# Optimization experiments

Measured on AMD Instinct MI355X. Metric: run time of the kernel, lower is better.

The kernel has to match this reference:

```python
import jax, jax.numpy as jnp
import numpy as np

D_IN = 1024
D_OUT = 1024
NUM_HEADS = 16
D_HEAD = D_OUT // NUM_HEADS


def setup_inputs() -> dict:
    key = jax.random.key(0)
    ks = jax.random.split(key, 6)
    s = 0.02
    return {
        "x": jax.random.normal(ks[0], (2, 2048, D_IN), dtype=jnp.float32),
        "W_q": jax.random.normal(ks[1], (D_IN, D_OUT), dtype=jnp.float32) * s,
        "W_k": jax.random.normal(ks[2], (D_IN, D_OUT), dtype=jnp.float32) * s,
        "W_v": jax.random.normal(ks[3], (D_IN, D_OUT), dtype=jnp.float32) * s,
        "W_o": jax.random.normal(ks[4], (D_OUT, D_OUT), dtype=jnp.float32) * s,
        "b_o": jax.random.normal(ks[5], (D_OUT,), dtype=jnp.float32) * s,
    }


def reference(x, W_q, W_k, W_v, W_o, b_o):
    B, T, _ = x.shape
    # qkv projections (no bias), split heads -> [B, H, T, d_head]
    def split_heads(t):
        return t.reshape(B, T, NUM_HEADS, D_HEAD).transpose(0, 2, 1, 3)
    q = split_heads(x @ W_q)
    k = split_heads(x @ W_k)
    v = split_heads(x @ W_v)
    # full causal scores [B, H, T, T]
    scores = jnp.einsum("bhqd,bhkd->bhqk", q, k)
    causal = jnp.triu(jnp.ones((T, T), dtype=bool), k=1)
    scores = jnp.where(causal, -jnp.inf, scores)
    attn = jax.nn.softmax(scores / np.sqrt(D_HEAD).astype(np.float32), axis=-1)
    # dropout rate is 0.0 -> identity
    ctx = jnp.einsum("bhqk,bhkd->bhqd", attn, v)
    ctx = ctx.transpose(0, 2, 1, 3).reshape(B, T, D_OUT)
    return ctx @ W_o + b_o
```

## Files before the change

kernel.cpp:

```cpp
#include <hip/hip_runtime.h>
#include <hip/hip_bf16.h>
#include <cstdint>

#define SEQ_T 2048
#define DMODEL 1024
#define NHEAD 16
#define DHEAD 64

typedef __attribute__((ext_vector_type(8))) __bf16 bf16x8;
typedef __attribute__((ext_vector_type(4))) float floatx4;

static __device__ __forceinline__ uint16_t f2bf(float f) {
    union { float f; uint32_t u; } v; v.f = f;
    uint32_t r = v.u + 0x7FFFu + ((v.u >> 16) & 1u);
    return (uint16_t)(r >> 16);
}

__global__ void mha_cvt_x(const float* __restrict__ x, uint16_t* __restrict__ xb) {
    int i = (blockIdx.x * blockDim.x + threadIdx.x) * 4;
    float4 f = *(const float4*)(x + i);
    union { uint16_t u[4]; uint64_t v; } o;
    o.u[0] = f2bf(f.x); o.u[1] = f2bf(f.y); o.u[2] = f2bf(f.z); o.u[3] = f2bf(f.w);
    *(uint64_t*)(xb + i) = o.v;
}

__global__ void mha_cvt_wt(const float* __restrict__ W0, const float* __restrict__ W1,
                           const float* __restrict__ W2, const float* __restrict__ W3,
                           uint16_t* __restrict__ T0, uint16_t* __restrict__ T1,
                           uint16_t* __restrict__ T2, uint16_t* __restrict__ T3) {
    const float* W; uint16_t* Tt;
    switch (blockIdx.z) {
        case 0: W = W0; Tt = T0; break;
        case 1: W = W1; Tt = T1; break;
        case 2: W = W2; Tt = T2; break;
        default: W = W3; Tt = T3; break;
    }
    __shared__ float tile[64][65];
    const int c  = threadIdx.x & 63;
    const int r0 = threadIdx.x >> 6;
    const int R0 = blockIdx.y * 64, C0 = blockIdx.x * 64;
#pragma unroll
    for (int rr = 0; rr < 16; ++rr) {
        int r = r0 + rr * 4;
        tile[r][c] = W[(size_t)(R0 + r) * DMODEL + C0 + c];
    }
    __syncthreads();
#pragma unroll
    for (int rr = 0; rr < 16; ++rr) {
        int r = r0 + rr * 4;
        Tt[(size_t)(C0 + r) * DMODEL + R0 + c] = f2bf(tile[c][r]);
    }
}

template<int MODE>
__device__ __forceinline__ void gemm128_body(
    const uint16_t* __restrict__ A, const uint16_t* __restrict__ Bt,
    uint16_t* __restrict__ outB) {
    const int K = DMODEL, N = DMODEL;
    __shared__ uint16_t As[128 * 32];
    __shared__ uint16_t Bs[128 * 32];
    const int tid  = threadIdx.x;
    const int wave = tid >> 6;
    const int lane = tid & 63;
    const int m0 = blockIdx.y * 128;
    const int n0 = blockIdx.x * 128;
    const int lr   = lane & 15;
    const int quad = lane >> 4;
    const int wm = wave >> 1, wn = wave & 1;

    floatx4 acc[4][4];
#pragma unroll
    for (int i = 0; i < 4; ++i)
#pragma unroll
        for (int j = 0; j < 4; ++j) acc[i][j] = (floatx4)0.0f;

    for (int k0 = 0; k0 < K; k0 += 32) {
#pragma unroll
        for (int i = 0; i < 2; ++i) {
            int chunk = i * 256 + wave * 64 + lane;
            int r  = chunk >> 2;
            int c8 = (chunk & 3) * 8;
            const uint16_t* ga = A  + (size_t)(m0 + r) * K + k0 + c8;
            const uint16_t* gb = Bt + (size_t)(n0 + r) * K + k0 + c8;
            uint16_t* la = &As[(size_t)(i * 256 + wave * 64) * 8];
            uint16_t* lb = &Bs[(size_t)(i * 256 + wave * 64) * 8];
            __builtin_amdgcn_global_load_lds((const __attribute__((address_space(1))) void*)ga,
                                             (__attribute__((address_space(3))) void*)la, 16, 0, 0);
            __builtin_amdgcn_global_load_lds((const __attribute__((address_space(1))) void*)gb,
                                             (__attribute__((address_space(3))) void*)lb, 16, 0, 0);
        }
        __syncthreads();
        bf16x8 af[4], bfr[4];
#pragma unroll
        for (int mi = 0; mi < 4; ++mi)
            af[mi] = *(const bf16x8*)&As[(wm * 64 + mi * 16 + lr) * 32 + quad * 8];
#pragma unroll
        for (int ni = 0; ni < 4; ++ni)
            bfr[ni] = *(const bf16x8*)&Bs[(wn * 64 + ni * 16 + lr) * 32 + quad * 8];
#pragma unroll
        for (int mi = 0; mi < 4; ++mi)
#pragma unroll
            for (int ni = 0; ni < 4; ++ni)
                acc[mi][ni] = __builtin_amdgcn_mfma_f32_16x16x32_bf16(af[mi], bfr[ni], acc[mi][ni], 0, 0, 0);
        __syncthreads();
    }
    if constexpr (MODE == 1) {
        __shared__ uint16_t Ct[64][136];
        const int bb = m0 >> 11;
        const int t0 = m0 & 2047;
#pragma unroll
        for (int p = 0; p < 2; ++p) {
            if (wn == p) {
#pragma unroll
                for (int mi = 0; mi < 4; ++mi)
#pragma unroll
                    for (int ni = 0; ni < 4; ++ni) {
                        int cl = ni * 16 + lr;
                        int tl = wm * 64 + mi * 16 + quad * 4;
                        union { uint16_t u[4]; uint64_t v8; } pk;
#pragma unroll
                        for (int r = 0; r < 4; ++r) pk.u[r] = f2bf(acc[mi][ni][r]);
                        *(uint64_t*)&Ct[cl][tl] = pk.v8;
                    }
            }
            __syncthreads();
#pragma unroll
            for (int k = 0; k < 4; ++k) {
                int c  = k * 256 + tid;
                int cl = c >> 4;
                int off = (c & 15) * 8;
                uint4 v = *(const uint4*)&Ct[cl][off];
                *(uint4*)&outB[((size_t)(bb * 1024 + n0 + p * 64 + cl)) * 2048 + t0 + off] = v;
            }
            __syncthreads();
        }
    } else {
#pragma unroll
        for (int mi = 0; mi < 4; ++mi)
#pragma unroll
            for (int ni = 0; ni < 4; ++ni) {
                int col = n0 + wn * 64 + ni * 16 + lr;
#pragma unroll
                for (int r = 0; r < 4; ++r) {
                    int row = m0 + wm * 64 + mi * 16 + quad * 4 + r;
                    outB[(size_t)row * N + col] = f2bf(acc[mi][ni][r]);
                }
            }
    }
}

__global__ __launch_bounds__(256) void mha_gemm_qkv(
    const uint16_t* __restrict__ A,
    const uint16_t* __restrict__ Wq, const uint16_t* __restrict__ Wk, const uint16_t* __restrict__ Wv,
    uint16_t* __restrict__ Q, uint16_t* __restrict__ K, uint16_t* __restrict__ Vt) {
    switch (blockIdx.z) {
        case 0:  gemm128_body<0>(A, Wq, Q);  break;
        case 1:  gemm128_body<0>(A, Wk, K);  break;
        default: gemm128_body<1>(A, Wv, Vt); break;
    }
}

__global__ __launch_bounds__(256) void mha_gemm_out(
    const uint16_t* __restrict__ A, const uint16_t* __restrict__ Wot,
    float* __restrict__ out, const float* __restrict__ bias) {
    const int K = DMODEL, N = DMODEL;
    __shared__ uint16_t As[128 * 32];
    __shared__ uint16_t Bs[64 * 32];
    const int tid  = threadIdx.x;
    const int wave = tid >> 6;
    const int lane = tid & 63;
    const int m0 = blockIdx.y * 128;
    const int n0 = blockIdx.x * 64;
    const int lr   = lane & 15;
    const int quad = lane >> 4;
    const int wm = wave >> 1, wn = wave & 1;

    floatx4 acc[4][2];
#pragma unroll
    for (int i = 0; i < 4; ++i)
#pragma unroll
        for (int j = 0; j < 2; ++j) acc[i][j] = (floatx4)0.0f;

    for (int k0 = 0; k0 < K; k0 += 32) {
#pragma unroll
        for (int i = 0; i < 2; ++i) {
            int chunk = i * 256 + wave * 64 + lane;
            int r  = chunk >> 2;
            int c8 = (chunk & 3) * 8;
            const uint16_t* ga = A + (size_t)(m0 + r) * K + k0 + c8;
            uint16_t* la = &As[(size_t)(i * 256 + wave * 64) * 8];
            __builtin_amdgcn_global_load_lds((const __attribute__((address_space(1))) void*)ga,
                                             (__attribute__((address_space(3))) void*)la, 16, 0, 0);
        }
        {
            int chunk = wave * 64 + lane;
            int r  = chunk >> 2;
            int c8 = (chunk & 3) * 8;
            const uint16_t* gb = Wot + (size_t)(n0 + r) * K + k0 + c8;
            uint16_t* lb = &Bs[(size_t)(wave * 64) * 8];
            __builtin_amdgcn_global_load_lds((const __attribute__((address_space(1))) void*)gb,
                                             (__attribute__((address_space(3))) void*)lb, 16, 0, 0);
        }
        __syncthreads();
        bf16x8 af[4], bfr[2];
#pragma unroll
        for (int mi = 0; mi < 4; ++mi)
            af[mi] = *(const bf16x8*)&As[(wm * 64 + mi * 16 + lr) * 32 + quad * 8];
#pragma unroll
        for (int ni = 0; ni < 2; ++ni)
            bfr[ni] = *(const bf16x8*)&Bs[(wn * 32 + ni * 16 + lr) * 32 + quad * 8];
#pragma unroll
        for (int mi = 0; mi < 4; ++mi)
#pragma unroll
            for (int ni = 0; ni < 2; ++ni)
                acc[mi][ni] = __builtin_amdgcn_mfma_f32_16x16x32_bf16(af[mi], bfr[ni], acc[mi][ni], 0, 0, 0);
        __syncthreads();
    }
#pragma unroll
    for (int mi = 0; mi < 4; ++mi)
#pragma unroll
        for (int ni = 0; ni < 2; ++ni) {
            int col = n0 + wn * 32 + ni * 16 + lr;
            float bv = bias[col];
#pragma unroll
            for (int r = 0; r < 4; ++r) {
                int row = m0 + wm * 64 + mi * 16 + quad * 4 + r;
                out[(size_t)row * N + col] = acc[mi][ni][r] + bv;
            }
        }
}

__global__ __launch_bounds__(256) void mha_attn_mfma(
    const uint16_t* __restrict__ Q, const uint16_t* __restrict__ K,
    const uint16_t* __restrict__ Vt, uint16_t* __restrict__ ctx) {
    __shared__ alignas(16) uint16_t Ks[2][64 * 64];
    __shared__ alignas(16) uint16_t Vs[2][64 * 64];
    __shared__ alignas(16) uint16_t Pb[64 * 72];

    const int tid  = threadIdx.x;
    const int wave = tid >> 6;
    const int lane = tid & 63;
    const int lr   = lane & 15;
    const int quad = lane >> 4;
    const int p  = blockIdx.x;
    const int h  = blockIdx.y;
    const int b  = blockIdx.z;
    const int jH = 31 - p, jL = p;
    const int TH = jH + 1;
    const int TL = jL + 1;
    const int Ttot = TH + TL;

    const uint16_t* kbase[2];
    const uint16_t* vbase[2];
#pragma unroll
    for (int i = 0; i < 2; ++i) {
        int c = i * 256 + tid;
        int row = c >> 3, cs = c & 7;
        int csk = cs ^ (row & 7);
        kbase[i] = K  + ((size_t)(b * SEQ_T) + row) * DMODEL + h * DHEAD + csk * 8;
        vbase[i] = Vt + ((size_t)(b * 1024 + h * DHEAD + row)) * 2048 + csk * 8;
    }

    int wrow = jH * 64 + wave * 16;
    bf16x8 qf0, qf1;
    {
        const size_t qb = ((size_t)(b * SEQ_T) + wrow + lr) * DMODEL + h * DHEAD;
        qf0 = *(const bf16x8*)(Q + qb + quad * 8);
        qf1 = *(const bf16x8*)(Q + qb + 32 + quad * 8);
    }
    floatx4 o[4];
#pragma unroll
    for (int nt = 0; nt < 4; ++nt) o[nt] = (floatx4)0.0f;
    float l[4] = {0.f, 0.f, 0.f, 0.f};

    auto stage = [&](int kv0, int buf) {
#pragma unroll
        for (int i = 0; i < 2; ++i) {
            const uint16_t* gk = kbase[i] + (size_t)kv0 * DMODEL;
            const uint16_t* gv = vbase[i] + kv0;
            uint16_t* lk = &Ks[buf][(i * 256 + wave * 64) * 8];
            uint16_t* lv = &Vs[buf][(i * 256 + wave * 64) * 8];
            __builtin_amdgcn_global_load_lds((const __attribute__((address_space(1))) void*)gk,
                                             (__attribute__((address_space(3))) void*)lk, 16, 0, 0);
            __builtin_amdgcn_global_load_lds((const __attribute__((address_space(1))) void*)gv,
                                             (__attribute__((address_space(3))) void*)lv, 16, 0, 0);
        }
    };
    auto epilogue = [&]() {
#pragma unroll
        for (int r = 0; r < 4; ++r) {
            float v = l[r];
            v += __shfl_xor(v, 1, 64);
            v += __shfl_xor(v, 2, 64);
            v += __shfl_xor(v, 4, 64);
            v += __shfl_xor(v, 8, 64);
            l[r] = 1.f / v;
        }
#pragma unroll
        for (int nt = 0; nt < 4; ++nt)
#pragma unroll
            for (int r = 0; r < 4; ++r) {
                size_t addr = ((size_t)(b * SEQ_T) + wrow + quad * 4 + r) * DMODEL + h * DHEAD + nt * 16 + lr;
                ctx[addr] = f2bf(o[nt][r] * l[r]);
            }
    };

    stage(0, 0);
    __syncthreads();
    int cur = 0;

    for (int t = 0; t < Ttot; ++t) {
        if (t + 1 < Ttot) {
            int nkv0 = ((t + 1 < TH) ? (t + 1) : (t + 1 - TH)) * 64;
            stage(nkv0, cur ^ 1);
        }
        const int kv0 = ((t < TH) ? t : (t - TH)) * 64;

        floatx4 s[4];
#pragma unroll
        for (int nt = 0; nt < 4; ++nt) {
            s[nt] = (floatx4)0.0f;
            int krow = nt * 16 + lr;
#pragma unroll
            for (int ks = 0; ks < 2; ++ks) {
                bf16x8 kf = *(const bf16x8*)&Ks[cur][krow * 64 + (((ks * 4 + quad) ^ (lr & 7)) * 8)];
                s[nt] = __builtin_amdgcn_mfma_f32_16x16x32_bf16(ks ? qf1 : qf0, kf, s[nt], 0, 0, 0);
            }
        }
        if (kv0 + 63 > wrow) {
#pragma unroll
            for (int nt = 0; nt < 4; ++nt) {
                int kcol = kv0 + nt * 16 + lr;
#pragma unroll
                for (int r = 0; r < 4; ++r) {
                    int qrow = wrow + quad * 4 + r;
                    if (kcol > qrow) s[nt][r] = -3e38f;
                }
            }
        }
#pragma unroll
        for (int nt = 0; nt < 4; ++nt)
#pragma unroll
            for (int r = 0; r < 4; ++r) {
                float pe = __expf(s[nt][r] * 0.125f);
                uint32_t pu = __float_as_uint(pe);
                l[r] += __uint_as_float(pu & 0xffff0000u);
                Pb[(wave * 16 + quad * 4 + r) * 72 + nt * 16 + lr] = (uint16_t)(pu >> 16);
            }
#pragma unroll
        for (int ks = 0; ks < 2; ++ks) {
            bf16x8 pfr = *(const bf16x8*)&Pb[(wave * 16 + lr) * 72 + ks * 32 + quad * 8];
#pragma unroll
            for (int nt = 0; nt < 4; ++nt) {
                int vrow = nt * 16 + lr;
                bf16x8 vf = *(const bf16x8*)&Vs[cur][vrow * 64 + (((ks * 4 + quad) ^ (lr & 7)) * 8)];
                o[nt] = __builtin_amdgcn_mfma_f32_16x16x32_bf16(pfr, vf, o[nt], 0, 0, 0);
            }
        }
        if (t == TH - 1) {
            epilogue();
            wrow = jL * 64 + wave * 16;
            const size_t qb = ((size_t)(b * SEQ_T) + wrow + lr) * DMODEL + h * DHEAD;
            qf0 = *(const bf16x8*)(Q + qb + quad * 8);
            qf1 = *(const bf16x8*)(Q + qb + 32 + quad * 8);
#pragma unroll
            for (int nt = 0; nt < 4; ++nt) o[nt] = (floatx4)0.0f;
#pragma unroll
            for (int r = 0; r < 4; ++r) l[r] = 0.f;
        }
        __syncthreads();
        cur ^= 1;
    }
    epilogue();
}

extern "C" void kernel_launch(void* const* d_in, const int* in_sizes, int n_in,
                              void* d_out, int out_size, void* d_ws, size_t ws_size,
                              hipStream_t stream) {
    const float* x  = (const float*)d_in[0];
    const float* Wq = (const float*)d_in[1];
    const float* Wk = (const float*)d_in[2];
    const float* Wv = (const float*)d_in[3];
    const float* Wo = (const float*)d_in[4];
    const float* bo = (const float*)d_in[5];
    float* out = (float*)d_out;

    char* ws = (char*)d_ws;
    const size_t SZ_X = (size_t)4096 * DMODEL * 2;
    const size_t SZ_W = (size_t)DMODEL * DMODEL * 2;
    size_t off = 0;
    uint16_t* xb  = (uint16_t*)(ws + off); off += SZ_X;
    uint16_t* wqt = (uint16_t*)(ws + off); off += SZ_W;
    uint16_t* wkt = (uint16_t*)(ws + off); off += SZ_W;
    uint16_t* wvt = (uint16_t*)(ws + off); off += SZ_W;
    uint16_t* wot = (uint16_t*)(ws + off); off += SZ_W;
    uint16_t* Qb  = (uint16_t*)(ws + off); off += SZ_X;
    uint16_t* Kb  = (uint16_t*)(ws + off); off += SZ_X;
    uint16_t* Vtb = (uint16_t*)(ws + off); off += SZ_X;
    uint16_t* Cb  = (uint16_t*)(ws + off); off += SZ_X;
    (void)ws_size; (void)in_sizes; (void)n_in; (void)out_size;

    mha_cvt_x<<<4096, 256, 0, stream>>>(x, xb);
    mha_cvt_wt<<<dim3(16, 16, 4), 256, 0, stream>>>(Wq, Wk, Wv, Wo, wqt, wkt, wvt, wot);
    mha_gemm_qkv<<<dim3(8, 32, 3), 256, 0, stream>>>(xb, wqt, wkt, wvt, Qb, Kb, Vtb);
    mha_attn_mfma<<<dim3(16, NHEAD, 2), 256, 0, stream>>>(Qb, Kb, Vtb, Cb);
    mha_gemm_out<<<dim3(16, 32), 256, 0, stream>>>(Cb, wot, out, bo);
}
```

Before: 201.6 us.

## Shrink GEMM tiles for more blocks, add LDS swizzle, reorder attention grid

Cuts the QKV projection tile to 64x128 and the output projection tile to 64x64, which doubles the block count so the 256 CUs are better filled. Adds an XOR swizzle to the LDS layouts to reduce bank conflicts on the MFMA fragment reads and the V-transpose staging. Swaps the attention grid axes so heads become the fastest-varying index, changing block scheduling order. Smaller tiles lower per-block data reuse and raise global and L2 traffic.

After: 198.6 us. About the same (-1.5%).

```diff
diff --git a/kernel.cpp b/kernel.cpp
--- a/kernel.cpp
+++ b/kernel.cpp
@@ -53,96 +53,98 @@
 }
 
 template<int MODE>
-__device__ __forceinline__ void gemm128_body(
+__device__ __forceinline__ void gemm64x128_body(
     const uint16_t* __restrict__ A, const uint16_t* __restrict__ Bt,
     uint16_t* __restrict__ outB) {
     const int K = DMODEL, N = DMODEL;
-    __shared__ uint16_t As[128 * 32];
-    __shared__ uint16_t Bs[128 * 32];
+    __shared__ alignas(16) char smem[(MODE == 1) ? 18432 : 12288];
+    uint16_t* As = (uint16_t*)smem;
+    uint16_t* Bs = (uint16_t*)(smem + 4096);
     const int tid  = threadIdx.x;
     const int wave = tid >> 6;
     const int lane = tid & 63;
-    const int m0 = blockIdx.y * 128;
+    const int m0 = blockIdx.y * 64;
     const int n0 = blockIdx.x * 128;
     const int lr   = lane & 15;
     const int quad = lane >> 4;
-    const int wm = wave >> 1, wn = wave & 1;
-
-    floatx4 acc[4][4];
+
+    floatx4 acc[4][2];
 #pragma unroll
     for (int i = 0; i < 4; ++i)
 #pragma unroll
-        for (int j = 0; j < 4; ++j) acc[i][j] = (floatx4)0.0f;
+        for (int j = 0; j < 2; ++j) acc[i][j] = (floatx4)0.0f;
 
     for (int k0 = 0; k0 < K; k0 += 32) {
 #pragma unroll
-        for (int i = 0; i < 2; ++i) {
-            int chunk = i * 256 + wave * 64 + lane;
-            int r  = chunk >> 2;
-            int c8 = (chunk & 3) * 8;
-            const uint16_t* ga = A  + (size_t)(m0 + r) * K + k0 + c8;
-            const uint16_t* gb = Bt + (size_t)(n0 + r) * K + k0 + c8;
-            uint16_t* la = &As[(size_t)(i * 256 + wave * 64) * 8];
-            uint16_t* lb = &Bs[(size_t)(i * 256 + wave * 64) * 8];
-            __builtin_amdgcn_global_load_lds((const __attribute__((address_space(1))) void*)ga,
-                                             (__attribute__((address_space(3))) void*)la, 16, 0, 0);
-            __builtin_amdgcn_global_load_lds((const __attribute__((address_space(1))) void*)gb,
-                                             (__attribute__((address_space(3))) void*)lb, 16, 0, 0);
-        }
-        __syncthreads();
-        bf16x8 af[4], bfr[4];
+        for (int it = 0; it < 3; ++it) {
+            int c = it * 256 + wave * 64 + lane;
+            if (it == 0) {
+                int r = c >> 2, s = (c & 3) ^ ((r >> 1) & 3);
+                const uint16_t* g = A + (size_t)(m0 + r) * K + k0 + s * 8;
+                uint16_t* l = As + (size_t)c * 8;
+                __builtin_amdgcn_global_load_lds((const __attribute__((address_space(1))) void*)g,
+                                                 (__attribute__((address_space(3))) void*)l, 16, 0, 0);
+            } else {
+                int j = c - 256;
+                int r = j >> 2, s = (j & 3) ^ ((r >> 1) & 3);
+                const uint16_t* g = Bt + (size_t)(n0 + r) * K + k0 + s * 8;
+                uint16_t* l = Bs + (size_t)j * 8;
+                __builtin_amdgcn_global_load_lds((const __attribute__((address_space(1))) void*)g,
+                                                 (__attribute__((address_space(3))) void*)l, 16, 0, 0);
+            }
+        }
+        __syncthreads();
+        bf16x8 af[4], bfr[2];
+#pragma unroll
+        for (int mi = 0; mi < 4; ++mi) {
+            int row = mi * 16 + lr;
+            af[mi] = *(const bf16x8*)&As[row * 32 + ((quad ^ ((row >> 1) & 3)) << 3)];
+        }
+#pragma unroll
+        for (int ni = 0; ni < 2; ++ni) {
+            int row = wave * 32 + ni * 16 + lr;
+            bfr[ni] = *(const bf16x8*)&Bs[row * 32 + ((quad ^ ((row >> 1) & 3)) << 3)];
+        }
 #pragma unroll
         for (int mi = 0; mi < 4; ++mi)
-            af[mi] = *(const bf16x8*)&As[(wm * 64 + mi * 16 + lr) * 32 + quad * 8];
-#pragma unroll
-        for (int ni = 0; ni < 4; ++ni)
-            bfr[ni] = *(const bf16x8*)&Bs[(wn * 64 + ni * 16 + lr) * 32 + quad * 8];
+#pragma unroll
+            for (int ni = 0; ni < 2; ++ni)
+                acc[mi][ni] = __builtin_amdgcn_mfma_f32_16x16x32_bf16(af[mi], bfr[ni], acc[mi][ni], 0, 0, 0);
+        __syncthreads();
+    }
+    if constexpr (MODE == 1) {
+        uint16_t* Ct = (uint16_t*)smem;
+        const int bb = m0 >> 11, t0 = m0 & 2047;
 #pragma unroll
         for (int mi = 0; mi < 4; ++mi)
 #pragma unroll
-            for (int ni = 0; ni < 4; ++ni)
-                acc[mi][ni] = __builtin_amdgcn_mfma_f32_16x16x32_bf16(af[mi], bfr[ni], acc[mi][ni], 0, 0, 0);
-        __syncthreads();
-    }
-    if constexpr (MODE == 1) {
-        __shared__ uint16_t Ct[64][136];
-        const int bb = m0 >> 11;
-        const int t0 = m0 & 2047;
-#pragma unroll
-        for (int p = 0; p < 2; ++p) {
-            if (wn == p) {
-#pragma unroll
-                for (int mi = 0; mi < 4; ++mi)
-#pragma unroll
-                    for (int ni = 0; ni < 4; ++ni) {
-                        int cl = ni * 16 + lr;
-                        int tl = wm * 64 + mi * 16 + quad * 4;
-                        union { uint16_t u[4]; uint64_t v8; } pk;
-#pragma unroll
-                        for (int r = 0; r < 4; ++r) pk.u[r] = f2bf(acc[mi][ni][r]);
-                        *(uint64_t*)&Ct[cl][tl] = pk.v8;
-                    }
-            }
-            __syncthreads();
-#pragma unroll
-            for (int k = 0; k < 4; ++k) {
-                int c  = k * 256 + tid;
-                int cl = c >> 4;
-                int off = (c & 15) * 8;
-                uint4 v = *(const uint4*)&Ct[cl][off];
-                *(uint4*)&outB[((size_t)(bb * 1024 + n0 + p * 64 + cl)) * 2048 + t0 + off] = v;
-            }
-            __syncthreads();
+            for (int ni = 0; ni < 2; ++ni) {
+                int cl = wave * 32 + ni * 16 + lr;
+                int tl = mi * 16 + quad * 4;
+                int tls = tl ^ ((cl & 3) << 4);
+                union { uint16_t u[4]; uint64_t v8; } pk;
+#pragma unroll
+                for (int r = 0; r < 4; ++r) pk.u[r] = f2bf(acc[mi][ni][r]);
+                *(uint64_t*)&Ct[cl * 72 + tls] = pk.v8;
+            }
+        __syncthreads();
+#pragma unroll
+        for (int k = 0; k < 4; ++k) {
+            int c = k * 256 + tid;
+            int cl = c >> 3, off = (c & 7) * 8;
+            int offs = off ^ ((cl & 3) << 4);
+            uint4 v = *(const uint4*)&Ct[cl * 72 + offs];
+            *(uint4*)&outB[((size_t)(bb * 1024 + n0 + cl)) * 2048 + t0 + off] = v;
         }
     } else {
 #pragma unroll
         for (int mi = 0; mi < 4; ++mi)
 #pragma unroll
-            for (int ni = 0; ni < 4; ++ni) {
-                int col = n0 + wn * 64 + ni * 16 + lr;
+            for (int ni = 0; ni < 2; ++ni) {
+                int col = n0 + wave * 32 + ni * 16 + lr;
 #pragma unroll
                 for (int r = 0; r < 4; ++r) {
-                    int row = m0 + wm * 64 + mi * 16 + quad * 4 + r;
+                    int row = m0 + mi * 16 + quad * 4 + r;
                     outB[(size_t)row * N + col] = f2bf(acc[mi][ni][r]);
                 }
             }
@@ -154,9 +156,9 @@
     const uint16_t* __restrict__ Wq, const uint16_t* __restrict__ Wk, const uint16_t* __restrict__ Wv,
     uint16_t* __restrict__ Q, uint16_t* __restrict__ K, uint16_t* __restrict__ Vt) {
     switch (blockIdx.z) {
-        case 0:  gemm128_body<0>(A, Wq, Q);  break;
-        case 1:  gemm128_body<0>(A, Wk, K);  break;
-        default: gemm128_body<1>(A, Wv, Vt); break;
+        case 0:  gemm64x128_body<0>(A, Wq, Q);  break;
+        case 1:  gemm64x128_body<0>(A, Wk, K);  break;
+        default: gemm64x128_body<1>(A, Wv, Vt); break;
     }
 }
 
@@ -164,69 +166,56 @@
     const uint16_t* __restrict__ A, const uint16_t* __restrict__ Wot,
     float* __restrict__ out, const float* __restrict__ bias) {
     const int K = DMODEL, N = DMODEL;
-    __shared__ uint16_t As[128 * 32];
-    __shared__ uint16_t Bs[64 * 32];
+    __shared__ alignas(16) uint16_t As[64 * 32];
+    __shared__ alignas(16) uint16_t Bs[64 * 32];
     const int tid  = threadIdx.x;
     const int wave = tid >> 6;
     const int lane = tid & 63;
-    const int m0 = blockIdx.y * 128;
+    const int m0 = blockIdx.y * 64;
     const int n0 = blockIdx.x * 64;
     const int lr   = lane & 15;
     const int quad = lane >> 4;
-    const int wm = wave >> 1, wn = wave & 1;
-
-    floatx4 acc[4][2];
-#pragma unroll
-    for (int i = 0; i < 4; ++i)
-#pragma unroll
-        for (int j = 0; j < 2; ++j) acc[i][j] = (floatx4)0.0f;
+
+    floatx4 acc[4];
+#pragma unroll
+    for (int i = 0; i < 4; ++i) acc[i] = (floatx4)0.0f;
 
     for (int k0 = 0; k0 < K; k0 += 32) {
 #pragma unroll
-        for (int i = 0; i < 2; ++i) {
-            int chunk = i * 256 + wave * 64 + lane;
-            int r  = chunk >> 2;
-            int c8 = (chunk & 3) * 8;
-            const uint16_t* ga = A + (size_t)(m0 + r) * K + k0 + c8;
-            uint16_t* la = &As[(size_t)(i * 256 + wave * 64) * 8];
-            __builtin_amdgcn_global_load_lds((const __attribute__((address_space(1))) void*)ga,
-                                             (__attribute__((address_space(3))) void*)la, 16, 0, 0);
+        for (int it = 0; it < 2; ++it) {
+            int c = it * 256 + wave * 64 + lane;
+            int j = c & 255;
+            int r = j >> 2, s = (j & 3) ^ ((r >> 1) & 3);
+            const uint16_t* g = (it == 0) ? (A   + (size_t)(m0 + r) * K + k0 + s * 8)
+                                          : (Wot + (size_t)(n0 + r) * K + k0 + s * 8);
+            uint16_t* l = ((it == 0) ? As : Bs) + (size_t)j * 8;
+            __builtin_amdgcn_global_load_lds((const __attribute__((address_space(1))) void*)g,
+                                             (__attribute__((address_space(3))) void*)l, 16, 0, 0);
+        }
+        __syncthreads();
+        bf16x8 af[4], bfr;
+#pragma unroll
+        for (int mi = 0; mi < 4; ++mi) {
+            int row = mi * 16 + lr;
+            af[mi] = *(const bf16x8*)&As[row * 32 + ((quad ^ ((row >> 1) & 3)) << 3)];
         }
         {
-            int chunk = wave * 64 + lane;
-            int r  = chunk >> 2;
-            int c8 = (chunk & 3) * 8;
-            const uint16_t* gb = Wot + (size_t)(n0 + r) * K + k0 + c8;
-            uint16_t* lb = &Bs[(size_t)(wave * 64) * 8];
-            __builtin_amdgcn_global_load_lds((const __attribute__((address_space(1))) void*)gb,
-                                             (__attribute__((address_space(3))) void*)lb, 16, 0, 0);
-        }
-        __syncthreads();
-        bf16x8 af[4], bfr[2];
+            int row = wave * 16 + lr;
+            bfr = *(const bf16x8*)&Bs[row * 32 + ((quad ^ ((row >> 1) & 3)) << 3)];
+        }
 #pragma unroll
         for (int mi = 0; mi < 4; ++mi)
-            af[mi] = *(const bf16x8*)&As[(wm * 64 + mi * 16 + lr) * 32 + quad * 8];
-#pragma unroll
-        for (int ni = 0; ni < 2; ++ni)
-            bfr[ni] = *(const bf16x8*)&Bs[(wn * 32 + ni * 16 + lr) * 32 + quad * 8];
-#pragma unroll
-        for (int mi = 0; mi < 4; ++mi)
-#pragma unroll
-            for (int ni = 0; ni < 2; ++ni)
-                acc[mi][ni] = __builtin_amdgcn_mfma_f32_16x16x32_bf16(af[mi], bfr[ni], acc[mi][ni], 0, 0, 0);
-        __syncthreads();
-    }
+            acc[mi] = __builtin_amdgcn_mfma_f32_16x16x32_bf16(af[mi], bfr, acc[mi], 0, 0, 0);
+        __syncthreads();
+    }
+    int col = n0 + wave * 16 + lr;
+    float bv = bias[col];
 #pragma unroll
     for (int mi = 0; mi < 4; ++mi)
 #pragma unroll
-        for (int ni = 0; ni < 2; ++ni) {
-            int col = n0 + wn * 32 + ni * 16 + lr;
-            float bv = bias[col];
-#pragma unroll
-            for (int r = 0; r < 4; ++r) {
-                int row = m0 + wm * 64 + mi * 16 + quad * 4 + r;
-                out[(size_t)row * N + col] = acc[mi][ni][r] + bv;
-            }
+        for (int r = 0; r < 4; ++r) {
+            int row = m0 + mi * 16 + quad * 4 + r;
+            out[(size_t)row * N + col] = acc[mi][r] + bv;
         }
 }
 
@@ -242,8 +231,8 @@
     const int lane = tid & 63;
     const int lr   = lane & 15;
     const int quad = lane >> 4;
-    const int p  = blockIdx.x;
-    const int h  = blockIdx.y;
+    const int h  = blockIdx.x;
+    const int p  = blockIdx.y;
     const int b  = blockIdx.z;
     const int jH = 31 - p, jL = p;
     const int TH = jH + 1;
@@ -402,7 +391,7 @@
 
     mha_cvt_x<<<4096, 256, 0, stream>>>(x, xb);
     mha_cvt_wt<<<dim3(16, 16, 4), 256, 0, stream>>>(Wq, Wk, Wv, Wo, wqt, wkt, wvt, wot);
-    mha_gemm_qkv<<<dim3(8, 32, 3), 256, 0, stream>>>(xb, wqt, wkt, wvt, Qb, Kb, Vtb);
-    mha_attn_mfma<<<dim3(16, NHEAD, 2), 256, 0, stream>>>(Qb, Kb, Vtb, Cb);
-    mha_gemm_out<<<dim3(16, 32), 256, 0, stream>>>(Cb, wot, out, bo);
-}
+    mha_gemm_qkv<<<dim3(8, 64, 3), 256, 0, stream>>>(xb, wqt, wkt, wvt, Qb, Kb, Vtb);
+    mha_attn_mfma<<<dim3(NHEAD, 16, 2), 256, 0, stream>>>(Qb, Kb, Vtb, Cb);
+    mha_gemm_out<<<dim3(16, 64), 256, 0, stream>>>(Cb, wot, out, bo);
+}
```
